# Kernel optimization log

Measured on AMD Instinct MI355X. Metric: run time of the kernel, lower is better.

Reference implementation:

```python
import jax, jax.numpy as jnp
import numpy as np

L = 8          # fixed number of instance labels (0 = background), all assumed present
DV = 0.5       # delta_v
DD = 1.5       # delta_d
LOSS_WEIGHT = 1.0


def _safe_norm(x, axis):
    sq = jnp.sum(x * x, axis=axis)
    pos = sq > 0
    return jnp.sqrt(jnp.where(pos, sq, 1.0)) * pos.astype(x.dtype)


def _per_image(emb, inst, kern, tmask):
    # emb: [D,H,W], inst: [H,W] int, kern/tmask: [H,W] float
    D, H, W = emb.shape
    HW = H * W
    tm = (tmask > 0.5).astype(inst.dtype)
    kb = (kern > 0.5).astype(inst.dtype)
    inst = inst * tm
    inst_k = (inst * kb).reshape(-1)          # kernel-region labels
    inst_f = inst.reshape(-1)                 # full-region labels
    emb_f = emb.reshape(D, -1).T              # [HW, D]

    # --- generate_coef: first/second occurrence (row-major) of each label ---
    flat = jnp.arange(HW)
    eq = inst_f[None, :] == jnp.arange(L)[:, None]          # [L, HW]
    idxs = jnp.where(eq, flat[None, :], HW)
    first = jnp.min(idxs, axis=1)
    second = jnp.min(jnp.where(idxs == first[:, None], HW, idxs), axis=1)
    first = jnp.minimum(first, HW - 1)
    second = jnp.minimum(second, HW - 1)
    r0, c0 = first // W, first % W
    r1, c1 = second // W, second % W
    # pos_id = (tmp[0,0], tmp[1,0], tmp[0,-1], tmp[1,-1]) as in the source
    pos = jnp.stack([r0, r1, c0, c1], axis=1).astype(jnp.float32)  # [L,4]
    diag = jnp.sqrt(jnp.float32(H * H + W * W))
    coef_diag = jnp.exp(jnp.sqrt((pos[:, 0] - pos[:, 2]) ** 2 +
                                 (pos[:, 1] - pos[:, 3]) ** 2) / diag / 2.0)
    zmask = (jnp.arange(L) > 0).astype(jnp.float32)          # skip label 0
    coef_diag = coef_diag * zmask
    s = pos[:, 0] + pos[:, 2]
    t = pos[:, 1] + pos[:, 3]
    dp = jnp.sqrt((s[:, None] - s[None, :]) ** 2 + (t[:, None] - t[None, :]) ** 2)
    coef_off = 1.0 - 20.0 * jnp.exp(-4.0 - 2.5 * dp / diag)
    eye = jnp.eye(L, dtype=bool)
    coef = jnp.where(eye, coef_diag[:, None], coef_off)
    coef = coef * zmask[:, None] * zmask[None, :]

    # --- per-label kernel means (segment mean) ---
    ones = jnp.ones((HW,), jnp.float32)
    cnt_k = jax.ops.segment_sum(ones, inst_k, num_segments=L)
    mean = jax.ops.segment_sum(emb_f, inst_k, num_segments=L)
    mean = mean / jnp.maximum(cnt_k, 1.0)[:, None]           # [L, D]
    mean = mean * zmask[:, None]

    # --- l_agg: per-pixel distance to own-label mean, segment-mean per label ---
    mean_px = mean[inst_f]                                   # [HW, D] gather
    dist = _safe_norm(emb_f - mean_px, axis=1)
    cd_px = coef_diag[inst_f]
    val = jnp.log(jax.nn.relu(cd_px * dist - DV) ** 2 + 1.0)
    cnt = jax.ops.segment_sum(ones, inst_f, num_segments=L)
    l_agg_per = jax.ops.segment_sum(val, inst_f, num_segments=L) / jnp.maximum(cnt, 1.0)
    l_agg = jnp.mean(l_agg_per[1:])

    # --- l_dis: coefficient-weighted pairwise hinge between means ---
    Dn = _safe_norm(mean[:, None, :] - mean[None, :, :], axis=-1)  # [L, L]
    pm = (~eye) & (zmask[:, None] > 0) & (zmask[None, :] > 0)
    vals = jnp.log(jax.nn.relu(2.0 * DD - coef * Dn) ** 2 + 1.0)
    l_dis = jnp.sum(jnp.where(pm, vals, 0.0)) / ((L - 1) * (L - 2))

    # --- l_reg ---
    l_reg = jnp.mean(jnp.log(_safe_norm(mean, axis=1) + 1.0)) * 0.001
    return l_agg + l_dis + l_reg


def reference(emb, instance, kernel, training_mask, bboxes):
    # bboxes is accepted but unused, matching the original forward_single
    loss_batch = jax.vmap(_per_image)(emb, instance, kernel, training_mask)
    return LOSS_WEIGHT * jnp.mean(loss_batch)


def setup_inputs() -> dict:
    key = jax.random.key(0)
    k1, k2, k3, k4, k5 = jax.random.split(key, 5)
    B, D, H, W = 8, 4, 640, 640
    emb = jax.random.normal(k1, (B, D, H, W), dtype=jnp.float32)
    instance = jax.random.randint(k2, (B, H, W), 0, L, dtype=jnp.int32)
    kernel = jax.random.uniform(k3, (B, H, W), dtype=jnp.float32)
    training_mask = jax.random.uniform(k4, (B, H, W), dtype=jnp.float32)
    bboxes = jax.random.uniform(k5, (B, 10, 4), dtype=jnp.float32)
    return {"emb": emb, "instance": instance, "kernel": kernel,
            "training_mask": training_mask, "bboxes": bboxes}
```

## Files before the change

### kernel.cpp

```cpp
#include <hip/hip_runtime.h>

#define B_    8
#define D_    4
#define H_    640
#define W_    640
#define HW_   (H_ * W_)
#define L_    8
#define NL    (L_ - 1)
#define BLOCK 256
#define VITER 2
#define PXB   (BLOCK * 4 * VITER)
#define GRIDX (HW_ / PXB)

__device__ __forceinline__ void gatom_add(float* p, float v) {
    unsafeAtomicAdd(p, v);
}

__global__ void k_init(int* ib) {
    int t = threadIdx.x;
    if (t < 128) ib[t] = HW_;
    ib[128 + t] = 0;
    if (t < 137) ib[384 + t] = 0;
}

__global__ __attribute__((amdgpu_flat_work_group_size(BLOCK, BLOCK),
                          amdgpu_waves_per_eu(4, 4)))
void k_pass1(
        const float* __restrict__ emb, const int* __restrict__ inst,
        const float* __restrict__ kern, const float* __restrict__ tmask,
        int* __restrict__ firstIdx, int* __restrict__ secondIdx,
        int* __restrict__ cntf_i, int* __restrict__ cntk_i,
        float* __restrict__ sumemb, unsigned int* __restrict__ lblpack) {
    __shared__ int   sCnt[L_];
    __shared__ float sSum[L_ * D_];
    __shared__ int   sM1[L_], sM2[L_];

    const int tid  = threadIdx.x;
    const int lane = tid & 63;
    if (tid < L_) { sCnt[tid] = 0; sM1[tid] = HW_; sM2[tid] = HW_; }
    if (tid < L_ * D_) sSum[tid] = 0.f;
    __syncthreads();

    const int b = blockIdx.y;
    const int blockbase = blockIdx.x * PXB;
    const float* embb = emb + (size_t)b * D_ * HW_;
    const int base = b * HW_;
    const int o0 = blockbase + tid * 4;

    int4 LB[2]; float4 TM[2], KN[2], E0[2], E1[2], E2[2], E3[2];
    {
        LB[0] = *(const int4*)  (inst  + base + o0);
        TM[0] = *(const float4*)(tmask + base + o0);
        KN[0] = *(const float4*)(kern  + base + o0);
        E0[0] = *(const float4*)(embb + 0 * HW_ + o0);
        E1[0] = *(const float4*)(embb + 1 * HW_ + o0);
        E2[0] = *(const float4*)(embb + 2 * HW_ + o0);
        E3[0] = *(const float4*)(embb + 3 * HW_ + o0);
    }

    float sm[NL][D_];
    #pragma unroll
    for (int l = 0; l < NL; ++l)
        #pragma unroll
        for (int d = 0; d < D_; ++d) sm[l][d] = 0.f;
    int bp0 = 0, bp1 = 0, bp2 = 0, km = 0;
    unsigned int lpLo = 0;

    #pragma unroll
    for (int it = 0; it < VITER; ++it) {
        const int cur = it & 1, nxt = cur ^ 1;
        if (it + 1 < VITER) {
            const int o = o0 + (it + 1) * (BLOCK * 4);
            LB[nxt] = *(const int4*)  (inst  + base + o);
            TM[nxt] = *(const float4*)(tmask + base + o);
            KN[nxt] = *(const float4*)(kern  + base + o);
            E0[nxt] = *(const float4*)(embb + 0 * HW_ + o);
            E1[nxt] = *(const float4*)(embb + 1 * HW_ + o);
            E2[nxt] = *(const float4*)(embb + 2 * HW_ + o);
            E3[nxt] = *(const float4*)(embb + 3 * HW_ + o);
        }
        const int*   labA = (const int*)&LB[cur];
        const float* tmA  = (const float*)&TM[cur];
        const float* knA  = (const float*)&KN[cur];
        const float* e0A  = (const float*)&E0[cur];
        const float* e1A  = (const float*)&E1[cur];
        const float* e2A  = (const float*)&E2[cur];
        const float* e3A  = (const float*)&E3[cur];

        #pragma unroll
        for (int c = 0; c < 4; ++c) {
            const int px = it * 4 + c;
            const int lf  = (tmA[c] > 0.5f) ? labA[c] : 0;
            const bool kb = (knA[c] > 0.5f);
            const int lfk = kb ? lf : 0;
            bp0 |= (lf & 1) << px;
            bp1 |= ((lf >> 1) & 1) << px;
            bp2 |= ((lf >> 2) & 1) << px;
            km  |= (kb ? 1 : 0) << px;
            lpLo |= (unsigned int)lf << (4 * px);
            #pragma unroll
            for (int l = 1; l < L_; ++l) {
                const float mk = (lfk == l) ? 1.0f : 0.0f;
                sm[l - 1][0] += mk * e0A[c];
                sm[l - 1][1] += mk * e1A[c];
                sm[l - 1][2] += mk * e2A[c];
                sm[l - 1][3] += mk * e3A[c];
            }
        }
    }

    lblpack[(size_t)(b * GRIDX + blockIdx.x) * BLOCK + tid] = lpLo;

    const int nb0 = ~bp0, nb1 = ~bp1, nb2 = ~bp2;
    int cnt[NL], m1[NL], m2[NL];
    #pragma unroll
    for (int l = 1; l < L_; ++l) {
        const int k = l - 1;
        int h = ((l & 1) ? bp0 : nb0) & ((l & 2) ? bp1 : nb1) & ((l & 4) ? bp2 : nb2);
        h &= 0xFF;
        cnt[k] = (__popc(h) << 16) | __popc(h & km);
        const int h2 = h & (h - 1);
        const int p1 = __ffs(h) - 1;
        const int p2 = __ffs(h2) - 1;
        m1[k] = h  ? (o0 + (p1 >> 2) * (BLOCK * 4) + (p1 & 3)) : HW_;
        m2[k] = h2 ? (o0 + (p2 >> 2) * (BLOCK * 4) + (p2 & 3)) : HW_;
    }

    #pragma unroll
    for (int l = 0; l < NL; ++l) {
        #pragma unroll
        for (int off = 32; off > 0; off >>= 1) {
            cnt[l]   += __shfl_down(cnt[l], off);
            sm[l][0] += __shfl_down(sm[l][0], off);
            sm[l][1] += __shfl_down(sm[l][1], off);
            sm[l][2] += __shfl_down(sm[l][2], off);
            sm[l][3] += __shfl_down(sm[l][3], off);
            int o1 = __shfl_down(m1[l], off);
            int o2 = __shfl_down(m2[l], off);
            m2[l] = min(min(m2[l], o2), max(m1[l], o1));
            m1[l] = min(m1[l], o1);
        }
    }
    if (lane == 0) {
        #pragma unroll
        for (int l = 0; l < NL; ++l) {
            atomicAdd(&sCnt[l + 1], cnt[l]);
            #pragma unroll
            for (int d = 0; d < D_; ++d) atomicAdd(&sSum[(l + 1) * D_ + d], sm[l][d]);
            int old = atomicMin(&sM1[l + 1], m1[l]);
            atomicMin(&sM2[l + 1], max(old, m1[l]));
            atomicMin(&sM2[l + 1], m2[l]);
        }
    }
    __syncthreads();

    if (tid >= 1 && tid < L_) {
        const int pc = sCnt[tid];
        atomicAdd(&cntf_i[b * L_ + tid], pc >> 16);
        atomicAdd(&cntk_i[b * L_ + tid], pc & 0xFFFF);
        int old = atomicMin(&firstIdx[b * L_ + tid], sM1[tid]);
        atomicMin(&secondIdx[b * L_ + tid], max(old, sM1[tid]));
        atomicMin(&secondIdx[b * L_ + tid], sM2[tid]);
    }
    if (tid >= D_ && tid < L_ * D_)
        gatom_add(&sumemb[b * L_ * D_ + tid], sSum[tid]);
}

__global__ __attribute__((amdgpu_flat_work_group_size(BLOCK, BLOCK),
                          amdgpu_waves_per_eu(8, 8)))
void k_pass3(
        const float* __restrict__ emb, const unsigned int* __restrict__ lblpack,
        const int* __restrict__ firstIdx, const int* __restrict__ secondIdx,
        const int* __restrict__ cntk_i, const int* __restrict__ cntf_i,
        const float* __restrict__ sumemb, float* __restrict__ sumvalb) {
    __shared__ float4 sMean[L_];
    __shared__ float  sCd[L_], sInv[L_];
    __shared__ float  sAcc;

    const int tid = threadIdx.x;
    const int b   = blockIdx.y;

    if (tid < L_) {
        float4 mu = {0.f, 0.f, 0.f, 0.f};
        float cd = 0.f, inv = 0.f;
        if (tid > 0) {
            const float invk = 1.0f / fmaxf((float)cntk_i[b * L_ + tid], 1.0f);
            mu.x = sumemb[b * L_ * D_ + tid * D_ + 0] * invk;
            mu.y = sumemb[b * L_ * D_ + tid * D_ + 1] * invk;
            mu.z = sumemb[b * L_ * D_ + tid * D_ + 2] * invk;
            mu.w = sumemb[b * L_ * D_ + tid * D_ + 3] * invk;
            const float diag = sqrtf((float)(H_ * H_ + W_ * W_));
            int f = min(firstIdx[b * L_ + tid],  HW_ - 1);
            int s = min(secondIdx[b * L_ + tid], HW_ - 1);
            float r0 = (float)(f / W_), c0 = (float)(f % W_);
            float r1 = (float)(s / W_), c1 = (float)(s % W_);
            cd = __expf(sqrtf((r0 - c0) * (r0 - c0) + (r1 - c1) * (r1 - c1))
                        / diag * 0.5f);
            inv = 1.0f / fmaxf((float)cntf_i[b * L_ + tid], 1.0f);
        }
        sMean[tid] = mu; sCd[tid] = cd; sInv[tid] = inv;
        if (tid == 0) sAcc = 0.f;
    }
    __syncthreads();

    const int blockbase = blockIdx.x * PXB;
    const float* embb = emb + (size_t)b * D_ * HW_;
    const int o0 = blockbase + tid * 4;

    const unsigned int lp = lblpack[(size_t)(b * GRIDX + blockIdx.x) * BLOCK + tid];
    float4 E[VITER][D_];
    #pragma unroll
    for (int it = 0; it < VITER; ++it)
        #pragma unroll
        for (int d = 0; d < D_; ++d)
            E[it][d] = *(const float4*)(embb + d * HW_ + o0 + it * (BLOCK * 4));

    float acc = 0.f;
    #pragma unroll
    for (int it = 0; it < VITER; ++it) {
        const float* e0A = (const float*)&E[it][0];
        const float* e1A = (const float*)&E[it][1];
        const float* e2A = (const float*)&E[it][2];
        const float* e3A = (const float*)&E[it][3];
        #pragma unroll
        for (int c = 0; c < 4; ++c) {
            const int px = it * 4 + c;
            const int lf = (int)((lp >> (4 * px)) & 7u);
            const float4 mu = sMean[lf];
            float dx = e0A[c] - mu.x, dy = e1A[c] - mu.y;
            float dz = e2A[c] - mu.z, dw = e3A[c] - mu.w;
            float d2 = dx * dx + dy * dy + dz * dz + dw * dw;
            float x  = fmaxf(sCd[lf] * sqrtf(d2) - 0.5f, 0.0f);
            acc += __logf(x * x + 1.0f) * sInv[lf];
        }
    }

    #pragma unroll
    for (int off = 32; off > 0; off >>= 1)
        acc += __shfl_down(acc, off);
    if ((tid & 63) == 0) atomicAdd(&sAcc, acc);
    __syncthreads();
    if (tid == 0) gatom_add(&sumvalb[b], sAcc);
}

__global__ __launch_bounds__(512) void k_final(
        const int* __restrict__ firstIdx, const int* __restrict__ secondIdx,
        const int* __restrict__ cntk_i, const float* __restrict__ sumemb,
        const float* __restrict__ sumvalb, float* __restrict__ out) {
    __shared__ float sWave[8];
    const int tid = threadIdx.x;
    const int b = tid >> 6, ij = tid & 63, i = ij >> 3, j = ij & 7;
    const float diag = sqrtf((float)(H_ * H_ + W_ * W_));

    float mi[D_], mj[D_];
    {
        float ci = 1.0f / fmaxf((float)cntk_i[b * L_ + i], 1.0f);
        float cj = 1.0f / fmaxf((float)cntk_i[b * L_ + j], 1.0f);
        #pragma unroll
        for (int d = 0; d < D_; ++d) {
            mi[d] = (i > 0) ? sumemb[(b * L_ + i) * D_ + d] * ci : 0.0f;
            mj[d] = (j > 0) ? sumemb[(b * L_ + j) * D_ + d] * cj : 0.0f;
        }
    }

    float contrib = 0.0f;
    if (j == 0) {
        float d2 = 0.f;
        #pragma unroll
        for (int d = 0; d < D_; ++d) d2 += mi[d] * mi[d];
        float n = (d2 > 0.f) ? sqrtf(d2) : 0.f;
        contrib += __logf(n + 1.0f) * (0.001f / (float)L_);
    }
    if (i == 0 && j == 1)
        contrib += sumvalb[b] * (1.0f / (float)NL);
    if (i >= 1 && j >= 1 && i != j) {
        float d2 = 0.f;
        #pragma unroll
        for (int d = 0; d < D_; ++d) {
            float df = mi[d] - mj[d];
            d2 += df * df;
        }
        float Dn = (d2 > 0.f) ? sqrtf(d2) : 0.f;
        int fi = min(firstIdx[b * L_ + i],  HW_ - 1);
        int si = min(secondIdx[b * L_ + i], HW_ - 1);
        int fj = min(firstIdx[b * L_ + j],  HW_ - 1);
        int sj = min(secondIdx[b * L_ + j], HW_ - 1);
        float ssi = (float)(fi / W_) + (float)(fi % W_);
        float tti = (float)(si / W_) + (float)(si % W_);
        float ssj = (float)(fj / W_) + (float)(fj % W_);
        float ttj = (float)(sj / W_) + (float)(sj % W_);
        float dx = ssi - ssj, dy = tti - ttj;
        float dp = sqrtf(dx * dx + dy * dy);
        float coef = 1.0f - 20.0f * __expf(-4.0f - 2.5f * dp / diag);
        float x = fmaxf(3.0f - coef * Dn, 0.0f);
        contrib += __logf(x * x + 1.0f) * (1.0f / 42.0f);
    }

    #pragma unroll
    for (int off = 32; off > 0; off >>= 1)
        contrib += __shfl_down(contrib, off);
    if ((tid & 63) == 0) sWave[tid >> 6] = contrib;
    __syncthreads();
    if (tid == 0) {
        float t = 0.f;
        #pragma unroll
        for (int w = 0; w < 8; ++w) t += sWave[w];
        out[0] = t * (1.0f / (float)B_);
    }
}

extern "C" void kernel_launch(void* const* d_in, const int* in_sizes, int n_in,
                              void* d_out, int out_size, void* d_ws, size_t ws_size,
                              hipStream_t stream) {
    const float* emb   = (const float*)d_in[0];
    const int*   inst  = (const int*)  d_in[1];
    const float* kern  = (const float*)d_in[2];
    const float* tmask = (const float*)d_in[3];

    int*   ib        = (int*)d_ws;
    int*   firstIdx  = ib;
    int*   secondIdx = ib + 64;
    int*   cntf_i    = ib + 128;
    int*   cntk_i    = ib + 192;
    float* sumemb    = (float*)(ib + 256);
    float* sumvalb   = (float*)(ib + 512);
    unsigned int* lblpack = (unsigned int*)(ib + 1024);
    float* out       = (float*)d_out;

    dim3 grid(GRIDX, B_);

    k_init <<<1, 256, 0, stream>>>(ib);
    k_pass1<<<grid, BLOCK, 0, stream>>>(emb, inst, kern, tmask,
                                        firstIdx, secondIdx, cntf_i, cntk_i,
                                        sumemb, lblpack);
    k_pass3<<<grid, BLOCK, 0, stream>>>(emb, lblpack, firstIdx, secondIdx,
                                        cntk_i, cntf_i, sumemb, sumvalb);
    k_final<<<1, 512, 0, stream>>>(firstIdx, secondIdx, cntk_i,
                                   sumemb, sumvalb, out);
}
```

Baseline: 170.4 us.

## Replace per-thread register accumulators with privatized LDS atomic histograms in pass1

Pass1 no longer keeps 28 per-thread float accumulators per label and reduces them with full-wave shuffles. Each thread now scatters embedding values, counts and first/second indices into 32-way privatized shared-memory bins using LDS atomics, and the bins are then reduced with 32-lane shuffles by 224 threads. This cuts register pressure and shuffle work, but adds LDS atomic contention and a larger shared-memory footprint. It also drops the double-buffered load loop in favour of issuing all loads up front, and relaxes the waves_per_eu bounds on both kernels.

New measurement: 213.7 us. 1.25x slower.

```diff
diff --git a/kernel.cpp b/kernel.cpp
--- a/kernel.cpp
+++ b/kernel.cpp
@@ -24,21 +24,25 @@
 }
 
 __global__ __attribute__((amdgpu_flat_work_group_size(BLOCK, BLOCK),
-                          amdgpu_waves_per_eu(4, 4)))
+                          amdgpu_waves_per_eu(4, 8)))
 void k_pass1(
         const float* __restrict__ emb, const int* __restrict__ inst,
         const float* __restrict__ kern, const float* __restrict__ tmask,
         int* __restrict__ firstIdx, int* __restrict__ secondIdx,
         int* __restrict__ cntf_i, int* __restrict__ cntk_i,
         float* __restrict__ sumemb, unsigned int* __restrict__ lblpack) {
-    __shared__ int   sCnt[L_];
-    __shared__ float sSum[L_ * D_];
-    __shared__ int   sM1[L_], sM2[L_];
-
-    const int tid  = threadIdx.x;
-    const int lane = tid & 63;
-    if (tid < L_) { sCnt[tid] = 0; sM1[tid] = HW_; sM2[tid] = HW_; }
-    if (tid < L_ * D_) sSum[tid] = 0.f;
+    __shared__ float        S [NL * 128];
+    __shared__ unsigned int C [NL * 32];
+    __shared__ int          M1[NL * 32], M2[NL * 32];
+
+    const int tid = threadIdx.x;
+    const int r   = tid & 31;
+
+    #pragma unroll
+    for (int i = tid; i < NL * 128 + NL * 32; i += BLOCK) {
+        if (i < NL * 128) S[i] = 0.f; else C[i - NL * 128] = 0u;
+    }
+    if (tid < NL * 32) { M1[tid] = HW_; M2[tid] = HW_; }
     __syncthreads();
 
     const int b = blockIdx.y;
@@ -47,64 +51,49 @@
     const int base = b * HW_;
     const int o0 = blockbase + tid * 4;
 
-    int4 LB[2]; float4 TM[2], KN[2], E0[2], E1[2], E2[2], E3[2];
-    {
-        LB[0] = *(const int4*)  (inst  + base + o0);
-        TM[0] = *(const float4*)(tmask + base + o0);
-        KN[0] = *(const float4*)(kern  + base + o0);
-        E0[0] = *(const float4*)(embb + 0 * HW_ + o0);
-        E1[0] = *(const float4*)(embb + 1 * HW_ + o0);
-        E2[0] = *(const float4*)(embb + 2 * HW_ + o0);
-        E3[0] = *(const float4*)(embb + 3 * HW_ + o0);
-    }
-
-    float sm[NL][D_];
-    #pragma unroll
-    for (int l = 0; l < NL; ++l)
-        #pragma unroll
-        for (int d = 0; d < D_; ++d) sm[l][d] = 0.f;
+    int4 LB[VITER]; float4 TM[VITER], KN[VITER];
+    float4 E0[VITER], E1[VITER], E2[VITER], E3[VITER];
+    #pragma unroll
+    for (int it = 0; it < VITER; ++it) {
+        const int o = o0 + it * (BLOCK * 4);
+        LB[it] = *(const int4*)  (inst  + base + o);
+        TM[it] = *(const float4*)(tmask + base + o);
+        KN[it] = *(const float4*)(kern  + base + o);
+        E0[it] = *(const float4*)(embb + 0 * HW_ + o);
+        E1[it] = *(const float4*)(embb + 1 * HW_ + o);
+        E2[it] = *(const float4*)(embb + 2 * HW_ + o);
+        E3[it] = *(const float4*)(embb + 3 * HW_ + o);
+    }
+
     int bp0 = 0, bp1 = 0, bp2 = 0, km = 0;
     unsigned int lpLo = 0;
 
     #pragma unroll
     for (int it = 0; it < VITER; ++it) {
-        const int cur = it & 1, nxt = cur ^ 1;
-        if (it + 1 < VITER) {
-            const int o = o0 + (it + 1) * (BLOCK * 4);
-            LB[nxt] = *(const int4*)  (inst  + base + o);
-            TM[nxt] = *(const float4*)(tmask + base + o);
-            KN[nxt] = *(const float4*)(kern  + base + o);
-            E0[nxt] = *(const float4*)(embb + 0 * HW_ + o);
-            E1[nxt] = *(const float4*)(embb + 1 * HW_ + o);
-            E2[nxt] = *(const float4*)(embb + 2 * HW_ + o);
-            E3[nxt] = *(const float4*)(embb + 3 * HW_ + o);
-        }
-        const int*   labA = (const int*)&LB[cur];
-        const float* tmA  = (const float*)&TM[cur];
-        const float* knA  = (const float*)&KN[cur];
-        const float* e0A  = (const float*)&E0[cur];
-        const float* e1A  = (const float*)&E1[cur];
-        const float* e2A  = (const float*)&E2[cur];
-        const float* e3A  = (const float*)&E3[cur];
-
+        const int*   labA = (const int*)&LB[it];
+        const float* tmA  = (const float*)&TM[it];
+        const float* knA  = (const float*)&KN[it];
+        const float* e0A  = (const float*)&E0[it];
+        const float* e1A  = (const float*)&E1[it];
+        const float* e2A  = (const float*)&E2[it];
+        const float* e3A  = (const float*)&E3[it];
         #pragma unroll
         for (int c = 0; c < 4; ++c) {
-            const int px = it * 4 + c;
+            const int px  = it * 4 + c;
             const int lf  = (tmA[c] > 0.5f) ? labA[c] : 0;
             const bool kb = (knA[c] > 0.5f);
-            const int lfk = kb ? lf : 0;
             bp0 |= (lf & 1) << px;
             bp1 |= ((lf >> 1) & 1) << px;
             bp2 |= ((lf >> 2) & 1) << px;
             km  |= (kb ? 1 : 0) << px;
             lpLo |= (unsigned int)lf << (4 * px);
-            #pragma unroll
-            for (int l = 1; l < L_; ++l) {
-                const float mk = (lfk == l) ? 1.0f : 0.0f;
-                sm[l - 1][0] += mk * e0A[c];
-                sm[l - 1][1] += mk * e1A[c];
-                sm[l - 1][2] += mk * e2A[c];
-                sm[l - 1][3] += mk * e3A[c];
+            const int lfk = kb ? lf : 0;
+            if (lfk > 0) {
+                float* p = &S[(lfk - 1) * 128 + r];
+                atomicAdd(p +  0, e0A[c]);
+                atomicAdd(p + 32, e1A[c]);
+                atomicAdd(p + 64, e2A[c]);
+                atomicAdd(p + 96, e3A[c]);
             }
         }
     }
@@ -112,62 +101,62 @@
     lblpack[(size_t)(b * GRIDX + blockIdx.x) * BLOCK + tid] = lpLo;
 
     const int nb0 = ~bp0, nb1 = ~bp1, nb2 = ~bp2;
-    int cnt[NL], m1[NL], m2[NL];
     #pragma unroll
     for (int l = 1; l < L_; ++l) {
-        const int k = l - 1;
         int h = ((l & 1) ? bp0 : nb0) & ((l & 2) ? bp1 : nb1) & ((l & 4) ? bp2 : nb2);
         h &= 0xFF;
-        cnt[k] = (__popc(h) << 16) | __popc(h & km);
-        const int h2 = h & (h - 1);
-        const int p1 = __ffs(h) - 1;
-        const int p2 = __ffs(h2) - 1;
-        m1[k] = h  ? (o0 + (p1 >> 2) * (BLOCK * 4) + (p1 & 3)) : HW_;
-        m2[k] = h2 ? (o0 + (p2 >> 2) * (BLOCK * 4) + (p2 & 3)) : HW_;
-    }
-
-    #pragma unroll
-    for (int l = 0; l < NL; ++l) {
-        #pragma unroll
-        for (int off = 32; off > 0; off >>= 1) {
-            cnt[l]   += __shfl_down(cnt[l], off);
-            sm[l][0] += __shfl_down(sm[l][0], off);
-            sm[l][1] += __shfl_down(sm[l][1], off);
-            sm[l][2] += __shfl_down(sm[l][2], off);
-            sm[l][3] += __shfl_down(sm[l][3], off);
-            int o1 = __shfl_down(m1[l], off);
-            int o2 = __shfl_down(m2[l], off);
-            m2[l] = min(min(m2[l], o2), max(m1[l], o1));
-            m1[l] = min(m1[l], o1);
-        }
-    }
-    if (lane == 0) {
-        #pragma unroll
-        for (int l = 0; l < NL; ++l) {
-            atomicAdd(&sCnt[l + 1], cnt[l]);
-            #pragma unroll
-            for (int d = 0; d < D_; ++d) atomicAdd(&sSum[(l + 1) * D_ + d], sm[l][d]);
-            int old = atomicMin(&sM1[l + 1], m1[l]);
-            atomicMin(&sM2[l + 1], max(old, m1[l]));
-            atomicMin(&sM2[l + 1], m2[l]);
-        }
-    }
-    __syncthreads();
-
-    if (tid >= 1 && tid < L_) {
-        const int pc = sCnt[tid];
-        atomicAdd(&cntf_i[b * L_ + tid], pc >> 16);
-        atomicAdd(&cntk_i[b * L_ + tid], pc & 0xFFFF);
-        int old = atomicMin(&firstIdx[b * L_ + tid], sM1[tid]);
-        atomicMin(&secondIdx[b * L_ + tid], max(old, sM1[tid]));
-        atomicMin(&secondIdx[b * L_ + tid], sM2[tid]);
-    }
-    if (tid >= D_ && tid < L_ * D_)
-        gatom_add(&sumemb[b * L_ * D_ + tid], sSum[tid]);
+        if (h) {
+            const int k32 = (l - 1) * 32 + r;
+            atomicAdd(&C[k32], ((unsigned int)__popc(h) << 16)
+                               | (unsigned int)__popc(h & km));
+            const int p1 = __ffs(h) - 1;
+            const int m1 = o0 + (p1 >> 2) * (BLOCK * 4) + (p1 & 3);
+            int old = atomicMin(&M1[k32], m1);
+            atomicMin(&M2[k32], max(old, m1));
+            const int h2 = h & (h - 1);
+            if (h2) {
+                const int p2 = __ffs(h2) - 1;
+                atomicMin(&M2[k32], o0 + (p2 >> 2) * (BLOCK * 4) + (p2 & 3));
+            }
+        }
+    }
+    __syncthreads();
+
+    if (tid < NL * 32) {
+        const int l  = tid >> 5;
+        const int rr = tid & 31;
+        const int s0 = l * 128 + rr;
+        float e0 = S[s0], e1 = S[s0 + 32], e2 = S[s0 + 64], e3 = S[s0 + 96];
+        unsigned int cc = C[l * 32 + rr];
+        int m1 = M1[l * 32 + rr], m2 = M2[l * 32 + rr];
+        #pragma unroll
+        for (int off = 16; off > 0; off >>= 1) {
+            e0 += __shfl_down(e0, off, 32);
+            e1 += __shfl_down(e1, off, 32);
+            e2 += __shfl_down(e2, off, 32);
+            e3 += __shfl_down(e3, off, 32);
+            cc += __shfl_down(cc, off, 32);
+            int o1 = __shfl_down(m1, off, 32);
+            int o2 = __shfl_down(m2, off, 32);
+            m2 = min(min(m2, o2), max(m1, o1));
+            m1 = min(m1, o1);
+        }
+        if (rr == 0) {
+            const int gl = b * L_ + (l + 1);
+            atomicAdd(&cntf_i[gl], (int)(cc >> 16));
+            atomicAdd(&cntk_i[gl], (int)(cc & 0xFFFFu));
+            int old = atomicMin(&firstIdx[gl], m1);
+            atomicMin(&secondIdx[gl], max(old, m1));
+            atomicMin(&secondIdx[gl], m2);
+            float* se = &sumemb[(size_t)gl * D_];
+            gatom_add(se + 0, e0); gatom_add(se + 1, e1);
+            gatom_add(se + 2, e2); gatom_add(se + 3, e3);
+        }
+    }
 }
 
 __global__ __attribute__((amdgpu_flat_work_group_size(BLOCK, BLOCK),
-                          amdgpu_waves_per_eu(8, 8)))
+                          amdgpu_waves_per_eu(4, 8)))
 void k_pass3(
         const float* __restrict__ emb, const unsigned int* __restrict__ lblpack,
         const int* __restrict__ firstIdx, const int* __restrict__ secondIdx,
```
